# Performance work log

Hardware: AMD Instinct MI355X
Metric: run time of the kernel (lower is better)

## Reference

```python
import jax, jax.numpy as jnp
import numpy as np

N, C, NE = 65536, 128, 10
INV_SQ2 = float(1.0 / np.sqrt(2.0))   # path weight sqrt(ir_out.dim / n_paths) * w3j, 0e outputs
INV_SQ6 = float(1.0 / np.sqrt(6.0))   # sqrt(1/2) * 1/sqrt(3) for the 1o.1o->0e dot path


def _fcn(x, weights):
    # e3nn FullyConnectedNet: no biases, fan-in normalized, silu between layers
    h = x
    for i, W in enumerate(weights):
        h = (h @ W) * float(1.0 / np.sqrt(W.shape[0]))
        if i < len(weights) - 1:
            h = jax.nn.silu(h)
    return h


def setup_inputs() -> dict:
    key = jax.random.key(0)
    ks = jax.random.split(key, 24)
    elem = jax.random.randint(ks[0], (N,), 0, NE)
    return {
        'node_feats_s': jax.random.normal(ks[1], (N, C), jnp.float32),
        'node_feats_v': jax.random.normal(ks[2], (N, C, 3), jnp.float32),
        'sc': jax.random.normal(ks[3], (N, 4 * C), jnp.float32),
        'node_attrs': jax.nn.one_hot(elem, NE, dtype=jnp.float32),
        'magmom_node_inv_feats': jax.random.normal(ks[4], (N, 16), jnp.float32),
        'magmom_node_attrs': jax.random.normal(ks[5], (N, 4), jnp.float32),
        'magmom_lenghts': jax.random.uniform(ks[6], (N, 1), jnp.float32),
        'Ws': jax.random.normal(ks[7], (NE, 5, C), jnp.float32),
        'Wv': jax.random.normal(ks[8], (NE, 4, C), jnp.float32),
        'Wc1': jax.random.normal(ks[9], (16, 64), jnp.float32),
        'Wc2': jax.random.normal(ks[10], (64, 64), jnp.float32),
        'Wc3': jax.random.normal(ks[11], (64, 64), jnp.float32),
        'Wc4': jax.random.normal(ks[12], (64, 4 * C), jnp.float32),
        'Wb1': jax.random.normal(ks[13], (16, 64), jnp.float32),
        'Wb2': jax.random.normal(ks[14], (64, 64), jnp.float32),
        'Wb3': jax.random.normal(ks[15], (64, 64), jnp.float32),
        'Wb4': jax.random.normal(ks[16], (64, C), jnp.float32),
        'exp_scaling': jnp.full((1,), 5.0, jnp.float32),
        'Wl0': jax.random.normal(ks[17], (2 * C, C), jnp.float32),
        'Wl1': jax.random.normal(ks[18], (2 * C, C), jnp.float32),
        'Wo0': jax.random.normal(ks[19], (C, C), jnp.float32),
        'Wo1': jax.random.normal(ks[20], (C, C), jnp.float32),
    }


def reference(node_feats_s, node_feats_v, sc, node_attrs, magmom_node_inv_feats,
              magmom_node_attrs, magmom_lenghts, Ws, Wv, Wc1, Wc2, Wc3, Wc4,
              Wb1, Wb2, Wb3, Wb4, exp_scaling, Wl0, Wl1, Wo0, Wo1):
    s, v = node_feats_s, node_feats_v                     # [N,C], [N,C,3]
    # --- SymmetricContraction (correlation 3, l<=1): per-element weighted symmetric CG basis ---
    ws = jnp.einsum('ne,epc->npc', node_attrs, Ws)        # [N,5,C] element-selected weights
    wv = jnp.einsum('ne,epc->npc', node_attrs, Wv)        # [N,4,C]
    vv = jnp.sum(v * v, axis=-1)                          # [N,C] invariant |v|^2
    out_s = (ws[:, 0] * s + ws[:, 1] * (s * s) + ws[:, 2] * vv
             + ws[:, 3] * (s * s * s) + ws[:, 4] * (s * vv))
    gate = wv[:, 0] + wv[:, 1] * s + wv[:, 2] * (s * s) + wv[:, 3] * vv
    out_v = gate[..., None] * v                           # [N,C,3] all 1o basis terms are multiples of v
    # --- conv_tp weights from invariant magmom feats ---
    tp_w = _fcn(magmom_node_inv_feats, [Wc1, Wc2, Wc3, Wc4])   # [N,4C]
    w0, w1, w2, w3 = (tp_w[:, 0:C], tp_w[:, C:2 * C], tp_w[:, 2 * C:3 * C], tp_w[:, 3 * C:4 * C])
    y0 = magmom_node_attrs[:, 0:1]                        # 1x0e
    y1 = magmom_node_attrs[:, 1:4]                        # 1x1o
    # --- path-sparse TensorProduct (uvu, per-sample weights), 4 instructions ---
    m0 = INV_SQ2 * w0 * out_s * y0                                     # 0e x 0e -> 0e
    m1 = INV_SQ6 * w1 * jnp.einsum('nci,ni->nc', out_v, y1)           # 1o x 1o -> 0e
    m2 = INV_SQ2 * w2[..., None] * out_s[..., None] * y1[:, None, :]  # 0e x 1o -> 1o
    m3 = INV_SQ2 * w3[..., None] * out_v * y0[:, :, None]             # 1o x 0e -> 1o
    # --- one-body magmom basis added to the scalar channels ---
    ob = _fcn(magmom_node_inv_feats, [Wb1, Wb2, Wb3, Wb4])            # [N,C]
    m0 = m0 + (1.0 - jnp.exp(-exp_scaling * magmom_lenghts)) * ob
    # --- equivariant Linear(irreps_mid -> target) + Linear(target -> target) + sc ---
    scal = jnp.concatenate([m0, m1], axis=1)              # [N,2C] 0e block
    vecs = jnp.concatenate([m2, m3], axis=1)              # [N,2C,3] 1o block
    inv_2c = float(1.0 / np.sqrt(2 * C))
    inv_c = float(1.0 / np.sqrt(C))
    out0 = (scal @ Wl0) * inv_2c
    out1 = jnp.einsum('nci,co->noi', vecs, Wl1) * inv_2c
    o0 = (out_s @ Wo0) * inv_c
    o1 = jnp.einsum('nci,co->noi', out_v, Wo1) * inv_c
    msg0 = out0 + o0 + sc[:, :C]
    msg1 = (out1 + o1).reshape(-1, 3 * C) + sc[:, C:]
    return jnp.concatenate([msg0, msg1], axis=1)          # [N, 4C] = target_irreps.dim
```

## Files before the change

### kernel.cpp

```cpp
#include <hip/hip_runtime.h>

#define NNODES 65536
#define CC 128
#define NEL 10
#define BN 32
#define NT 256

#define INV_SQ2f 0.70710678118654752440f
#define INV_SQ6f 0.40824829046386301637f
#define INV_2Cf  0.0625f
#define INV_Cf   0.08838834764831845f
#define S16f 0.25f
#define S64f 0.125f

#define WS_FRAGS 312
#define WS_BYTES (WS_FRAGS * 1024)

typedef __attribute__((ext_vector_type(8))) short s16x8;
typedef __attribute__((ext_vector_type(4))) float f32x4;
#define MFMA16(a, b, c) __builtin_amdgcn_mfma_f32_16x16x32_bf16((a), (b), (c), 0, 0, 0)

union U8 { unsigned short u[8]; s16x8 s; };

__device__ __forceinline__ unsigned short bf16rne(float x) {
    unsigned int u = __float_as_uint(x);
    return (unsigned short)((u + 0x7FFFu + ((u >> 16) & 1u)) >> 16);
}
__device__ __forceinline__ float bf2f(unsigned short h) {
    return __uint_as_float(((unsigned int)h) << 16);
}
__device__ __forceinline__ unsigned int packbf(float a, float b) {
    return (unsigned int)bf16rne(a) | (((unsigned int)bf16rne(b)) << 16);
}
__device__ __forceinline__ float siluf(float x) {
    return x * (1.0f / (1.0f + __expf(-x)));
}

extern "C" __global__ void prep_frags(
    const float* __restrict__ WC1, const float* __restrict__ WC2,
    const float* __restrict__ WC3, const float* __restrict__ WB1,
    const float* __restrict__ WB2, const float* __restrict__ WB3,
    const float* __restrict__ WC4, const float* __restrict__ WB4,
    const float* __restrict__ WL0, const float* __restrict__ WO0,
    const float* __restrict__ WL1, const float* __restrict__ WO1,
    unsigned short* __restrict__ wsb)
{
    const int b = blockIdx.x;
    const int l = threadIdx.x;
    const float* W; int K, N, nKS, base; float sc;
    if      (b <  4) { W = WC1; K = 16;  N = 64;  nKS = 1; base = 0;   sc = S16f; }
    else if (b < 12) { W = WC2; K = 64;  N = 64;  nKS = 2; base = 4;   sc = S64f; }
    else if (b < 20) { W = WC3; K = 64;  N = 64;  nKS = 2; base = 12;  sc = S64f; }
    else if (b < 24) { W = WB1; K = 16;  N = 64;  nKS = 1; base = 20;  sc = S16f; }
    else if (b < 32) { W = WB2; K = 64;  N = 64;  nKS = 2; base = 24;  sc = S64f; }
    else if (b < 40) { W = WB3; K = 64;  N = 64;  nKS = 2; base = 32;  sc = S64f; }
    else if (b < 104){ W = WC4; K = 64;  N = 512; nKS = 2; base = 40;  sc = S64f; }
    else if (b < 120){ W = WB4; K = 64;  N = 128; nKS = 2; base = 104; sc = S64f; }
    else if (b < 184){ W = WL0; K = 256; N = 128; nKS = 8; base = 120; sc = INV_2Cf; }
    else if (b < 216){ W = WO0; K = 128; N = 128; nKS = 4; base = 184; sc = INV_Cf; }
    else if (b < 280){ W = WL1; K = 256; N = 128; nKS = 8; base = 216; sc = INV_2Cf; }
    else             { W = WO1; K = 128; N = 128; nKS = 4; base = 280; sc = INV_Cf; }
    const int f  = b - base;
    const int nt = f / nKS, ks = f % nKS;
    const int n  = nt * 16 + (l & 15);
    const int k0 = ks * 32 + (l >> 4) * 8;
    U8 v;
    #pragma unroll
    for (int j = 0; j < 8; ++j) {
        const int k = k0 + j;
        const float x = (k < K) ? W[(size_t)k * N + n] * sc : 0.0f;
        v.u[j] = bf16rne(x);
    }
    *(s16x8*)(wsb + (size_t)b * 512 + l * 8) = v.s;
}

__device__ __forceinline__ s16x8 ldB(const unsigned short* __restrict__ wsb, int fragidx, int lane) {
    return *(const s16x8*)(wsb + ((size_t)fragidx << 9) + lane * 8);
}
__device__ __forceinline__ s16x8 ldA136(const unsigned short* X, int row, int ks, int gq) {
    return *(const s16x8*)(X + row * 136 + ks * 32 + gq * 8);
}
__device__ __forceinline__ s16x8 ldA72(const unsigned short* X, int row, int ks, int gq) {
    return *(const s16x8*)(X + row * 72 + ks * 32 + gq * 8);
}

extern "C" __global__ void __launch_bounds__(NT)
epb_mfma(const float* __restrict__ Sin, const float* __restrict__ Vin,
         const float* __restrict__ SCp, const float* __restrict__ ATT,
         const float* __restrict__ INVF, const float* __restrict__ MNA,
         const float* __restrict__ MLEN, const float* __restrict__ WSp,
         const float* __restrict__ WVp, const float* __restrict__ ESC,
         const unsigned short* __restrict__ wsb, float* __restrict__ OUT)
{
    extern __shared__ char smem[];
    unsigned short* B1 = (unsigned short*)smem;
    unsigned short* B2 = B1 + 4352;
    unsigned short* B3 = B2 + 4352;
    unsigned short* B4 = B3 + 4352;
    unsigned short* B5 = B4 + 4352;
    unsigned short* B6 = B5 + 4352;
    float* y0f  = (float*)(smem + 6 * 8704);
    float* y1f  = y0f + 32;
    float* etf  = y1f + 96;
    int*   eidx = (int*)(etf + 32);

    const int tid  = threadIdx.x;
    const int n0   = blockIdx.x * BN;
    const int w    = tid >> 6;
    const int lane = tid & 63;
    const int cl   = lane & 15;
    const int gq   = lane >> 4;
    const f32x4 Z4 = {0.f, 0.f, 0.f, 0.f};

    U8 invu[2];
    #pragma unroll
    for (int rg = 0; rg < 2; ++rg) {
        if (gq < 2) {
            const float* ip = INVF + (size_t)(n0 + rg * 16 + cl) * 16 + gq * 8;
            #pragma unroll
            for (int j = 0; j < 8; ++j) invu[rg].u[j] = bf16rne(ip[j]);
        } else {
            #pragma unroll
            for (int j = 0; j < 8; ++j) invu[rg].u[j] = 0;
        }
    }

    if (tid < BN) {
        const int gn = n0 + tid;
        y0f[tid] = MNA[gn * 4 + 0];
        y1f[tid * 3 + 0] = MNA[gn * 4 + 1];
        y1f[tid * 3 + 1] = MNA[gn * 4 + 2];
        y1f[tid * 3 + 2] = MNA[gn * 4 + 3];
        etf[tid] = 1.0f - __expf(-ESC[0] * MLEN[gn]);
        int e = 0;
        #pragma unroll
        for (int k = 0; k < NEL; ++k)
            if (ATT[(size_t)gn * NEL + k] > 0.5f) e = k;
        eidx[tid] = e;
    }

    #pragma unroll
    for (int rg = 0; rg < 2; ++rg) {
        const f32x4 c = MFMA16(invu[rg].s, ldB(wsb, 0 + w, lane), Z4);
        const f32x4 b = MFMA16(invu[rg].s, ldB(wsb, 20 + w, lane), Z4);
        #pragma unroll
        for (int r = 0; r < 4; ++r) {
            const int rw = rg * 16 + gq * 4 + r;
            B1[rw * 72 + w * 16 + cl] = bf16rne(siluf(c[r]));
            B2[rw * 72 + w * 16 + cl] = bf16rne(siluf(b[r]));
        }
    }
    __syncthreads();

    {
        f32x4 c[2] = {Z4, Z4}, b[2] = {Z4, Z4};
        #pragma unroll
        for (int ks = 0; ks < 2; ++ks) {
            const s16x8 fc = ldB(wsb, 4 + w * 2 + ks, lane);
            const s16x8 fb = ldB(wsb, 24 + w * 2 + ks, lane);
            #pragma unroll
            for (int rg = 0; rg < 2; ++rg) {
                c[rg] = MFMA16(ldA72(B1, rg * 16 + cl, ks, gq), fc, c[rg]);
                b[rg] = MFMA16(ldA72(B2, rg * 16 + cl, ks, gq), fb, b[rg]);
            }
        }
        #pragma unroll
        for (int rg = 0; rg < 2; ++rg)
            #pragma unroll
            for (int r = 0; r < 4; ++r) {
                const int rw = rg * 16 + gq * 4 + r;
                B3[rw * 72 + w * 16 + cl] = bf16rne(siluf(c[rg][r]));
                B4[rw * 72 + w * 16 + cl] = bf16rne(siluf(b[rg][r]));
            }
    }
    __syncthreads();

    {
        f32x4 c[2] = {Z4, Z4}, b[2] = {Z4, Z4};
        #pragma unroll
        for (int ks = 0; ks < 2; ++ks) {
            const s16x8 fc = ldB(wsb, 12 + w * 2 + ks, lane);
            const s16x8 fb = ldB(wsb, 32 + w * 2 + ks, lane);
            #pragma unroll
            for (int rg = 0; rg < 2; ++rg) {
                c[rg] = MFMA16(ldA72(B3, rg * 16 + cl, ks, gq), fc, c[rg]);
                b[rg] = MFMA16(ldA72(B4, rg * 16 + cl, ks, gq), fb, b[rg]);
            }
        }
        #pragma unroll
        for (int rg = 0; rg < 2; ++rg)
            #pragma unroll
            for (int r = 0; r < 4; ++r) {
                const int rw = rg * 16 + gq * 4 + r;
                B5[rw * 72 + w * 16 + cl] = bf16rne(siluf(c[rg][r]));
                B6[rw * 72 + w * 16 + cl] = bf16rne(siluf(b[rg][r]));
            }
    }
    __syncthreads();

    s16x8 h3c[2][2], h3b[2][2];
    #pragma unroll
    for (int rg = 0; rg < 2; ++rg)
        #pragma unroll
        for (int ks = 0; ks < 2; ++ks) {
            h3c[rg][ks] = ldA72(B5, rg * 16 + cl, ks, gq);
            h3b[rg][ks] = ldA72(B6, rg * 16 + cl, ks, gq);
        }
    f32x4 obacc[2][2];
    #pragma unroll
    for (int tc = 0; tc < 2; ++tc) {
        const int T = w * 2 + tc;
        const s16x8 f0 = ldB(wsb, 104 + T * 2 + 0, lane);
        const s16x8 f1 = ldB(wsb, 104 + T * 2 + 1, lane);
        #pragma unroll
        for (int rg = 0; rg < 2; ++rg)
            obacc[rg][tc] = MFMA16(h3b[rg][1], f1, MFMA16(h3b[rg][0], f0, Z4));
    }

    unsigned int vpack[3][8];
    {
        const int row = tid >> 3;
        const int c0  = (tid & 7) << 4;
        const size_t gn = (size_t)(n0 + row);
        const float4 mna = *(const float4*)(MNA + gn * 4);
        const float y10 = mna.y, y11 = mna.z, y12 = mna.w;
        int e = 0;
        #pragma unroll
        for (int k = 0; k < NEL; ++k)
            if (ATT[gn * NEL + k] > 0.5f) e = k;
        const float* sp  = Sin + gn * CC + c0;
        const float* vp  = Vin + (gn * CC + c0) * 3;
        const float* wsp = WSp + ((size_t)e * 5) * CC + c0;
        const float* wvp = WVp + ((size_t)e * 4) * CC + c0;
        unsigned int* B1d = (unsigned int*)B1;
        unsigned int* B2d = (unsigned int*)B2;
        unsigned int* B3d = (unsigned int*)B3;
        const int dbase = row * 68 + (c0 >> 1);
        #pragma unroll
        for (int jp = 0; jp < 8; ++jp) {
            const int c = 2 * jp;
            const float2 s2 = *(const float2*)(sp + c);
            const float2 va = *(const float2*)(vp + 3 * c);
            const float2 vb = *(const float2*)(vp + 3 * c + 2);
            const float2 vc = *(const float2*)(vp + 3 * c + 4);
            vpack[0][jp] = packbf(va.x, vb.y);
            vpack[1][jp] = packbf(va.y, vc.x);
            vpack[2][jp] = packbf(vb.x, vc.y);
            const float vv0 = va.x * va.x + va.y * va.y + vb.x * vb.x;
            const float vv1 = vb.y * vb.y + vc.x * vc.x + vc.y * vc.y;
            const float vy0 = va.x * y10 + va.y * y11 + vb.x * y12;
            const float vy1 = vb.y * y10 + vc.x * y11 + vc.y * y12;
            const float2 p0 = *(const float2*)(wsp + 0 * CC + c);
            const float2 p1 = *(const float2*)(wsp + 1 * CC + c);
            const float2 p2 = *(const float2*)(wsp + 2 * CC + c);
            const float2 p3 = *(const float2*)(wsp + 3 * CC + c);
            const float2 p4 = *(const float2*)(wsp + 4 * CC + c);
            const float2 q0 = *(const float2*)(wvp + 0 * CC + c);
            const float2 q1 = *(const float2*)(wvp + 1 * CC + c);
            const float2 q2 = *(const float2*)(wvp + 2 * CC + c);
            const float2 q3 = *(const float2*)(wvp + 3 * CC + c);
            const float s0 = s2.x, s1 = s2.y;
            const float ss0 = s0 * s0, ss1 = s1 * s1;
            const float os0 = p0.x * s0 + p1.x * ss0 + p2.x * vv0 + p3.x * (ss0 * s0) + p4.x * (s0 * vv0);
            const float os1 = p0.y * s1 + p1.y * ss1 + p2.y * vv1 + p3.y * (ss1 * s1) + p4.y * (s1 * vv1);
            const float gt0 = q0.x + q1.x * s0 + q2.x * ss0 + q3.x * vv0;
            const float gt1 = q0.y + q1.y * s1 + q2.y * ss1 + q3.y * vv1;
            B1d[dbase + jp] = packbf(os0, os1);
            B2d[dbase + jp] = packbf(gt0, gt1);
            B3d[dbase + jp] = packbf(vy0, vy1);
        }
    }
    __syncthreads();

#define WCHUNK(q, wc)                                                          \
    {                                                                          \
        _Pragma("unroll")                                                      \
        for (int tc = 0; tc < 2; ++tc) {                                       \
            const int T = w * 2 + tc;                                          \
            const s16x8 f0 = ldB(wsb, 40 + ((q) * 8 + T) * 2 + 0, lane);       \
            const s16x8 f1 = ldB(wsb, 40 + ((q) * 8 + T) * 2 + 1, lane);       \
            _Pragma("unroll")                                                  \
            for (int rg = 0; rg < 2; ++rg)                                     \
                wc[rg][tc] = MFMA16(h3c[rg][1], f1, MFMA16(h3c[rg][0], f0, Z4)); \
        }                                                                      \
    }
    {
        f32x4 wc[2][2];
        WCHUNK(0, wc)
        #pragma unroll
        for (int rg = 0; rg < 2; ++rg)
            #pragma unroll
            for (int tc = 0; tc < 2; ++tc)
                #pragma unroll
                for (int r = 0; r < 4; ++r) {
                    const int rw = rg * 16 + gq * 4 + r;
                    const int col = (w * 2 + tc) * 16 + cl;
                    const float os = bf2f(B1[rw * 136 + col]);
                    B4[rw * 136 + col] = bf16rne(INV_SQ2f * wc[rg][tc][r] * os * y0f[rw]
                                                 + etf[rw] * obacc[rg][tc][r]);
                }
        WCHUNK(1, wc)
        #pragma unroll
        for (int rg = 0; rg < 2; ++rg)
            #pragma unroll
            for (int tc = 0; tc < 2; ++tc)
                #pragma unroll
                for (int r = 0; r < 4; ++r) {
                    const int rw = rg * 16 + gq * 4 + r;
                    const int col = (w * 2 + tc) * 16 + cl;
                    const float gt = bf2f(B2[rw * 136 + col]);
                    const float vy = bf2f(B3[rw * 136 + col]);
                    B3[rw * 136 + col] = bf16rne(INV_SQ6f * wc[rg][tc][r] * gt * vy);
                }
        WCHUNK(2, wc)
        #pragma unroll
        for (int rg = 0; rg < 2; ++rg)
            #pragma unroll
            for (int tc = 0; tc < 2; ++tc)
                #pragma unroll
                for (int r = 0; r < 4; ++r) {
                    const int rw = rg * 16 + gq * 4 + r;
                    const int col = (w * 2 + tc) * 16 + cl;
                    B6[rw * 136 + col] = bf16rne(INV_SQ2f * wc[rg][tc][r] * bf2f(B1[rw * 136 + col]));
                }
        WCHUNK(3, wc)
        #pragma unroll
        for (int rg = 0; rg < 2; ++rg)
            #pragma unroll
            for (int tc = 0; tc < 2; ++tc)
                #pragma unroll
                for (int r = 0; r < 4; ++r) {
                    const int rw = rg * 16 + gq * 4 + r;
                    const int col = (w * 2 + tc) * 16 + cl;
                    const float gt = bf2f(B2[rw * 136 + col]);
                    B5[rw * 136 + col] = bf16rne(INV_SQ2f * wc[rg][tc][r] * gt * y0f[rw]);
                }
    }
#undef WCHUNK
    __syncthreads();

    f32x4 tacc[2][2] = {{Z4, Z4}, {Z4, Z4}};
    {
        f32x4 acc[2][2] = {{Z4, Z4}, {Z4, Z4}};
        #pragma unroll
        for (int ks = 0; ks < 12; ++ks) {
            const unsigned short* Xa = (ks < 4) ? B4 : (ks < 8) ? B3 : B1;
            s16x8 a[2];
            #pragma unroll
            for (int rg = 0; rg < 2; ++rg) a[rg] = ldA136(Xa, rg * 16 + cl, ks & 3, gq);
            #pragma unroll
            for (int tc = 0; tc < 2; ++tc) {
                const int T = w * 2 + tc;
                const int fi = (ks < 8) ? (120 + T * 8 + ks) : (184 + T * 4 + (ks - 8));
                const s16x8 bfrag = ldB(wsb, fi, lane);
                #pragma unroll
                for (int rg = 0; rg < 2; ++rg)
                    acc[rg][tc] = MFMA16(a[rg], bfrag, acc[rg][tc]);
            }
        }
        #pragma unroll
        for (int ks = 0; ks < 4; ++ks) {
            s16x8 a[2];
            #pragma unroll
            for (int rg = 0; rg < 2; ++rg) a[rg] = ldA136(B6, rg * 16 + cl, ks, gq);
            #pragma unroll
            for (int tc = 0; tc < 2; ++tc) {
                const s16x8 bfrag = ldB(wsb, 216 + (w * 2 + tc) * 8 + ks, lane);
                #pragma unroll
                for (int rg = 0; rg < 2; ++rg)
                    tacc[rg][tc] = MFMA16(a[rg], bfrag, tacc[rg][tc]);
            }
        }
        #pragma unroll
        for (int rg = 0; rg < 2; ++rg)
            #pragma unroll
            for (int tc = 0; tc < 2; ++tc)
                #pragma unroll
                for (int r = 0; r < 4; ++r) {
                    const int rw = rg * 16 + gq * 4 + r;
                    const size_t o = (size_t)(n0 + rw) * 512 + (w * 2 + tc) * 16 + cl;
                    OUT[o] = acc[rg][tc][r] + SCp[o];
                }
    }
    __syncthreads();

    f32x4 acc3[3][2][2];

#define STAGE_I(i, DSTB, DSTG)                                                  \
    {                                                                           \
        const int dbase = (tid >> 3) * 68 + (tid & 7) * 8;                      \
        const unsigned int* bD = (const unsigned int*)B5;                       \
        const unsigned int* gD = (const unsigned int*)B2;                       \
        unsigned int* o1 = (unsigned int*)(DSTB);                               \
        unsigned int* o3 = (unsigned int*)(DSTG);                               \
        _Pragma("unroll")                                                       \
        for (int jp = 0; jp < 8; ++jp) {                                        \
            const unsigned int bd = bD[dbase + jp];                             \
            const unsigned int gd = gD[dbase + jp];                             \
            const float v0 = bf2f((unsigned short)(vpack[i][jp] & 0xffff));     \
            const float v1 = bf2f((unsigned short)(vpack[i][jp] >> 16));        \
            o1[dbase + jp] = packbf(bf2f((unsigned short)(bd & 0xffff)) * v0,   \
                                    bf2f((unsigned short)(bd >> 16)) * v1);     \
            o3[dbase + jp] = packbf(bf2f((unsigned short)(gd & 0xffff)) * v0,   \
                                    bf2f((unsigned short)(gd >> 16)) * v1);     \
        }                                                                       \
    }

#define GEMM_I(i, SRCB, SRCG)                                                   \
    {                                                                           \
        _Pragma("unroll")                                                       \
        for (int rg = 0; rg < 2; ++rg)                                          \
            _Pragma("unroll")                                                   \
            for (int tc = 0; tc < 2; ++tc) acc3[i][rg][tc] = Z4;                \
        _Pragma("unroll")                                                       \
        for (int ks = 0; ks < 4; ++ks) {                                        \
            s16x8 a1[2], a3[2];                                                 \
            _Pragma("unroll")                                                   \
            for (int rg = 0; rg < 2; ++rg) {                                    \
                a1[rg] = ldA136((SRCB), rg * 16 + cl, ks, gq);                  \
                a3[rg] = ldA136((SRCG), rg * 16 + cl, ks, gq);                  \
            }                                                                   \
            _Pragma("unroll")                                                   \
            for (int tc = 0; tc < 2; ++tc) {                                    \
                const int T = w * 2 + tc;                                       \
                const s16x8 fb = ldB(wsb, 216 + T * 8 + 4 + ks, lane);          \
                const s16x8 fg = ldB(wsb, 280 + T * 4 + ks, lane);              \
                _Pragma("unroll")                                               \
                for (int rg = 0; rg < 2; ++rg) {                                \
                    acc3[i][rg][tc] = MFMA16(a1[rg], fb, acc3[i][rg][tc]);      \
                    acc3[i][rg][tc] = MFMA16(a3[rg], fg, acc3[i][rg][tc]);      \
                }                                                               \
            }                                                                   \
        }                                                                       \
    }

    STAGE_I(0, B1, B3)
    __syncthreads();
    GEMM_I(0, B1, B3)
    STAGE_I(1, B4, B6)
    __syncthreads();
    GEMM_I(1, B4, B6)
    STAGE_I(2, B1, B3)
    __syncthreads();
    GEMM_I(2, B1, B3)

    #pragma unroll
    for (int rg = 0; rg < 2; ++rg)
        #pragma unroll
        for (int tc = 0; tc < 2; ++tc)
            #pragma unroll
            for (int r = 0; r < 4; ++r) {
                const int rw = rg * 16 + gq * 4 + r;
                const int col = (w * 2 + tc) * 16 + cl;
                const size_t o = (size_t)(n0 + rw) * 512 + 128 + (size_t)col * 3;
                const float tv = tacc[rg][tc][r];
                OUT[o + 0] = acc3[0][rg][tc][r] + tv * y1f[rw * 3 + 0] + SCp[o + 0];
                OUT[o + 1] = acc3[1][rg][tc][r] + tv * y1f[rw * 3 + 1] + SCp[o + 1];
                OUT[o + 2] = acc3[2][rg][tc][r] + tv * y1f[rw * 3 + 2] + SCp[o + 2];
            }
#undef STAGE_I
#undef GEMM_I
}

extern "C" void kernel_launch(void* const* d_in, const int* in_sizes, int n_in,
                              void* d_out, int out_size, void* d_ws, size_t ws_size,
                              hipStream_t stream)
{
    (void)in_sizes; (void)n_in; (void)out_size; (void)ws_size;
    const float* Sin  = (const float*)d_in[0];
    const float* Vin  = (const float*)d_in[1];
    const float* SCp  = (const float*)d_in[2];
    const float* ATT  = (const float*)d_in[3];
    const float* INVF = (const float*)d_in[4];
    const float* MNA  = (const float*)d_in[5];
    const float* MLEN = (const float*)d_in[6];
    const float* WSp  = (const float*)d_in[7];
    const float* WVp  = (const float*)d_in[8];
    const float* WC1  = (const float*)d_in[9];
    const float* WC2  = (const float*)d_in[10];
    const float* WC3  = (const float*)d_in[11];
    const float* WC4  = (const float*)d_in[12];
    const float* WB1  = (const float*)d_in[13];
    const float* WB2  = (const float*)d_in[14];
    const float* WB3  = (const float*)d_in[15];
    const float* WB4  = (const float*)d_in[16];
    const float* ESC  = (const float*)d_in[17];
    const float* WL0  = (const float*)d_in[18];
    const float* WL1  = (const float*)d_in[19];
    const float* WO0  = (const float*)d_in[20];
    const float* WO1  = (const float*)d_in[21];
    float* OUT = (float*)d_out;

    unsigned short* wsb = (unsigned short*)d_ws;
    hipLaunchKernelGGL(prep_frags, dim3(WS_FRAGS), dim3(64), 0, stream,
                       WC1, WC2, WC3, WB1, WB2, WB3, WC4, WB4,
                       WL0, WO0, WL1, WO1, wsb);
    const size_t shbytes = (size_t)(6 * 8704 + 768);
    hipLaunchKernelGGL(epb_mfma, dim3(NNODES / BN), dim3(NT), shbytes, stream,
                       Sin, Vin, SCp, ATT, INVF, MNA, MLEN, WSp, WVp, ESC,
                       wsb, OUT);
}
```

Measured before the change: 166.4 us.

## Split the magmom MLP into a separate kernel writing h3 to workspace

Moves the two 3-layer radial/one-body MLPs out of the main fused kernel into a new mlp_h3 kernel. It runs one wave per 16 nodes with per-wave ping-pong LDS and no block barriers, and writes bf16 hidden activations to global workspace. The main kernel then loads h3 from global memory instead of computing it, which removes three __syncthreads phases and their LDS traffic. In exchange it adds an extra launch and about 16 MB of global write plus read, and it falls back to the old fused kernel when the workspace is too small.

```diff
diff --git a/kernel.cpp b/kernel.cpp
--- a/kernel.cpp
+++ b/kernel.cpp
@@ -14,7 +14,8 @@
 #define S64f 0.125f
 
 #define WS_FRAGS 312
-#define WS_BYTES (WS_FRAGS * 1024)
+#define H3_OFF   (WS_FRAGS * 512)
+#define WS_NEED  ((size_t)H3_OFF * 2 + (size_t)NNODES * 128 * 2)
 
 typedef __attribute__((ext_vector_type(8))) short s16x8;
 typedef __attribute__((ext_vector_type(4))) float f32x4;
@@ -84,13 +85,79 @@
     return *(const s16x8*)(X + row * 72 + ks * 32 + gq * 8);
 }
 
+extern "C" __global__ void __launch_bounds__(256)
+mlp_h3(const float* __restrict__ INVF, const unsigned short* __restrict__ wsb,
+       unsigned short* __restrict__ h3g)
+{
+    extern __shared__ unsigned short slab_all[];
+    const int tid  = threadIdx.x;
+    const int v    = tid >> 6;
+    const int lane = tid & 63;
+    const int cl   = lane & 15;
+    const int gq   = lane >> 4;
+    const int nbase = blockIdx.x * 64 + v * 16;
+    unsigned short* ping = slab_all + v * 2560;
+    unsigned short* pong = ping + 1280;
+    const f32x4 Z4 = {0.f, 0.f, 0.f, 0.f};
+
+    U8 invu;
+    if (gq < 2) {
+        const float* ip = INVF + (size_t)(nbase + cl) * 16 + gq * 8;
+        #pragma unroll
+        for (int j = 0; j < 8; ++j) invu.u[j] = bf16rne(ip[j]);
+    } else {
+        #pragma unroll
+        for (int j = 0; j < 8; ++j) invu.u[j] = 0;
+    }
+
+    #pragma unroll
+    for (int ch = 0; ch < 2; ++ch) {
+        #pragma unroll
+        for (int mt = 0; mt < 4; ++mt) {
+            const f32x4 c = MFMA16(invu.s, ldB(wsb, (ch ? 20 : 0) + mt, lane), Z4);
+            #pragma unroll
+            for (int r = 0; r < 4; ++r)
+                ping[(gq * 4 + r) * 80 + mt * 16 + cl] = bf16rne(siluf(c[r]));
+        }
+        #pragma unroll
+        for (int mt = 0; mt < 4; ++mt) {
+            f32x4 c = Z4;
+            #pragma unroll
+            for (int ks = 0; ks < 2; ++ks)
+                c = MFMA16(*(const s16x8*)(ping + cl * 80 + ks * 32 + gq * 8),
+                           ldB(wsb, (ch ? 24 : 4) + mt * 2 + ks, lane), c);
+            #pragma unroll
+            for (int r = 0; r < 4; ++r)
+                pong[(gq * 4 + r) * 80 + mt * 16 + cl] = bf16rne(siluf(c[r]));
+        }
+        #pragma unroll
+        for (int mt = 0; mt < 4; ++mt) {
+            f32x4 c = Z4;
+            #pragma unroll
+            for (int ks = 0; ks < 2; ++ks)
+                c = MFMA16(*(const s16x8*)(pong + cl * 80 + ks * 32 + gq * 8),
+                           ldB(wsb, (ch ? 32 : 12) + mt * 2 + ks, lane), c);
+            #pragma unroll
+            for (int r = 0; r < 4; ++r)
+                ping[(gq * 4 + r) * 80 + mt * 16 + cl] = bf16rne(siluf(c[r]));
+        }
+        #pragma unroll
+        for (int it = 0; it < 2; ++it) {
+            const int idx = it * 64 + lane;
+            const int row = idx >> 3, seg = idx & 7;
+            *(s16x8*)(h3g + (size_t)(nbase + row) * 128 + ch * 64 + seg * 8) =
+                *(const s16x8*)(ping + row * 80 + seg * 8);
+        }
+    }
+}
+
 extern "C" __global__ void __launch_bounds__(NT)
-epb_mfma(const float* __restrict__ Sin, const float* __restrict__ Vin,
+epb_lean(const float* __restrict__ Sin, const float* __restrict__ Vin,
          const float* __restrict__ SCp, const float* __restrict__ ATT,
-         const float* __restrict__ INVF, const float* __restrict__ MNA,
-         const float* __restrict__ MLEN, const float* __restrict__ WSp,
-         const float* __restrict__ WVp, const float* __restrict__ ESC,
-         const unsigned short* __restrict__ wsb, float* __restrict__ OUT)
+         const float* __restrict__ MNA, const float* __restrict__ MLEN,
+         const float* __restrict__ WSp, const float* __restrict__ WVp,
+         const float* __restrict__ ESC, const unsigned short* __restrict__ wsb,
+         const unsigned short* __restrict__ h3g, float* __restrict__ OUT)
 {
     extern __shared__ char smem[];
     unsigned short* B1 = (unsigned short*)smem;
@@ -102,7 +169,6 @@
     float* y0f  = (float*)(smem + 6 * 8704);
     float* y1f  = y0f + 32;
     float* etf  = y1f + 96;
-    int*   eidx = (int*)(etf + 32);
 
     const int tid  = threadIdx.x;
     const int n0   = blockIdx.x * BN;
@@ -112,19 +178,6 @@
     const int gq   = lane >> 4;
     const f32x4 Z4 = {0.f, 0.f, 0.f, 0.f};
 
-    U8 invu[2];
-    #pragma unroll
-    for (int rg = 0; rg < 2; ++rg) {
-        if (gq < 2) {
-            const float* ip = INVF + (size_t)(n0 + rg * 16 + cl) * 16 + gq * 8;
-            #pragma unroll
-            for (int j = 0; j < 8; ++j) invu[rg].u[j] = bf16rne(ip[j]);
-        } else {
-            #pragma unroll
-            for (int j = 0; j < 8; ++j) invu[rg].u[j] = 0;
-        }
-    }
-
     if (tid < BN) {
         const int gn = n0 + tid;
         y0f[tid] = MNA[gn * 4 + 0];
@@ -132,79 +185,16 @@
         y1f[tid * 3 + 1] = MNA[gn * 4 + 2];
         y1f[tid * 3 + 2] = MNA[gn * 4 + 3];
         etf[tid] = 1.0f - __expf(-ESC[0] * MLEN[gn]);
-        int e = 0;
-        #pragma unroll
-        for (int k = 0; k < NEL; ++k)
-            if (ATT[(size_t)gn * NEL + k] > 0.5f) e = k;
-        eidx[tid] = e;
-    }
-
-    #pragma unroll
-    for (int rg = 0; rg < 2; ++rg) {
-        const f32x4 c = MFMA16(invu[rg].s, ldB(wsb, 0 + w, lane), Z4);
-        const f32x4 b = MFMA16(invu[rg].s, ldB(wsb, 20 + w, lane), Z4);
-        #pragma unroll
-        for (int r = 0; r < 4; ++r) {
-            const int rw = rg * 16 + gq * 4 + r;
-            B1[rw * 72 + w * 16 + cl] = bf16rne(siluf(c[r]));
-            B2[rw * 72 + w * 16 + cl] = bf16rne(siluf(b[r]));
-        }
-    }
-    __syncthreads();
-
-    {
-        f32x4 c[2] = {Z4, Z4}, b[2] = {Z4, Z4};
+    }
+
+    s16x8 h3c[2][2], h3b[2][2];
+    #pragma unroll
+    for (int rg = 0; rg < 2; ++rg)
         #pragma unroll
         for (int ks = 0; ks < 2; ++ks) {
-            const s16x8 fc = ldB(wsb, 4 + w * 2 + ks, lane);
-            const s16x8 fb = ldB(wsb, 24 + w * 2 + ks, lane);
-            #pragma unroll
-            for (int rg = 0; rg < 2; ++rg) {
-                c[rg] = MFMA16(ldA72(B1, rg * 16 + cl, ks, gq), fc, c[rg]);
-                b[rg] = MFMA16(ldA72(B2, rg * 16 + cl, ks, gq), fb, b[rg]);
-            }
-        }
-        #pragma unroll
-        for (int rg = 0; rg < 2; ++rg)
-            #pragma unroll
-            for (int r = 0; r < 4; ++r) {
-                const int rw = rg * 16 + gq * 4 + r;
-                B3[rw * 72 + w * 16 + cl] = bf16rne(siluf(c[rg][r]));
-                B4[rw * 72 + w * 16 + cl] = bf16rne(siluf(b[rg][r]));
-            }
-    }
-    __syncthreads();
-
-    {
-        f32x4 c[2] = {Z4, Z4}, b[2] = {Z4, Z4};
-        #pragma unroll
-        for (int ks = 0; ks < 2; ++ks) {
-            const s16x8 fc = ldB(wsb, 12 + w * 2 + ks, lane);
-            const s16x8 fb = ldB(wsb, 32 + w * 2 + ks, lane);
-            #pragma unroll
-            for (int rg = 0; rg < 2; ++rg) {
-                c[rg] = MFMA16(ldA72(B3, rg * 16 + cl, ks, gq), fc, c[rg]);
-                b[rg] = MFMA16(ldA72(B4, rg * 16 + cl, ks, gq), fb, b[rg]);
-            }
-        }
-        #pragma unroll
-        for (int rg = 0; rg < 2; ++rg)
-            #pragma unroll
-            for (int r = 0; r < 4; ++r) {
-                const int rw = rg * 16 + gq * 4 + r;
-                B5[rw * 72 + w * 16 + cl] = bf16rne(siluf(c[rg][r]));
-                B6[rw * 72 + w * 16 + cl] = bf16rne(siluf(b[rg][r]));
-            }
-    }
-    __syncthreads();
-
-    s16x8 h3c[2][2], h3b[2][2];
-    #pragma unroll
-    for (int rg = 0; rg < 2; ++rg)
-        #pragma unroll
-        for (int ks = 0; ks < 2; ++ks) {
-            h3c[rg][ks] = ldA72(B5, rg * 16 + cl, ks, gq);
-            h3b[rg][ks] = ldA72(B6, rg * 16 + cl, ks, gq);
+            const size_t base = (size_t)(n0 + rg * 16 + cl) * 128 + ks * 32 + gq * 8;
+            h3c[rg][ks] = *(const s16x8*)(h3g + base);
+            h3b[rg][ks] = *(const s16x8*)(h3g + base + 64);
         }
     f32x4 obacc[2][2];
     #pragma unroll
@@ -462,11 +452,370 @@
 #undef GEMM_I
 }
 
+extern "C" __global__ void __launch_bounds__(NT)
+epb_mfma(const float* __restrict__ Sin, const float* __restrict__ Vin,
+         const float* __restrict__ SCp, const float* __restrict__ ATT,
+         const float* __restrict__ INVF, const float* __restrict__ MNA,
+         const float* __restrict__ MLEN, const float* __restrict__ WSp,
+         const float* __restrict__ WVp, const float* __restrict__ ESC,
+         const unsigned short* __restrict__ wsb, float* __restrict__ OUT)
+{
+    extern __shared__ char smem[];
+    unsigned short* B1 = (unsigned short*)smem;
+    unsigned short* B2 = B1 + 4352;
+    unsigned short* B3 = B2 + 4352;
+    unsigned short* B4 = B3 + 4352;
+    unsigned short* B5 = B4 + 4352;
+    unsigned short* B6 = B5 + 4352;
+    float* y0f  = (float*)(smem + 6 * 8704);
+    float* y1f  = y0f + 32;
+    float* etf  = y1f + 96;
+
+    const int tid  = threadIdx.x;
+    const int n0   = blockIdx.x * BN;
+    const int w    = tid >> 6;
+    const int lane = tid & 63;
+    const int cl   = lane & 15;
+    const int gq   = lane >> 4;
+    const f32x4 Z4 = {0.f, 0.f, 0.f, 0.f};
+
+    U8 invu[2];
+    #pragma unroll
+    for (int rg = 0; rg < 2; ++rg) {
+        if (gq < 2) {
+            const float* ip = INVF + (size_t)(n0 + rg * 16 + cl) * 16 + gq * 8;
+            #pragma unroll
+            for (int j = 0; j < 8; ++j) invu[rg].u[j] = bf16rne(ip[j]);
+        } else {
+            #pragma unroll
+            for (int j = 0; j < 8; ++j) invu[rg].u[j] = 0;
+        }
+    }
+    if (tid < BN) {
+        const int gn = n0 + tid;
+        y0f[tid] = MNA[gn * 4 + 0];
+        y1f[tid * 3 + 0] = MNA[gn * 4 + 1];
+        y1f[tid * 3 + 1] = MNA[gn * 4 + 2];
+        y1f[tid * 3 + 2] = MNA[gn * 4 + 3];
+        etf[tid] = 1.0f - __expf(-ESC[0] * MLEN[gn]);
+    }
+    #pragma unroll
+    for (int rg = 0; rg < 2; ++rg) {
+        const f32x4 c = MFMA16(invu[rg].s, ldB(wsb, 0 + w, lane), Z4);
+        const f32x4 b = MFMA16(invu[rg].s, ldB(wsb, 20 + w, lane), Z4);
+        #pragma unroll
+        for (int r = 0; r < 4; ++r) {
+            const int rw = rg * 16 + gq * 4 + r;
+            B1[rw * 72 + w * 16 + cl] = bf16rne(siluf(c[r]));
+            B2[rw * 72 + w * 16 + cl] = bf16rne(siluf(b[r]));
+        }
+    }
+    __syncthreads();
+    {
+        f32x4 c[2] = {Z4, Z4}, b[2] = {Z4, Z4};
+        #pragma unroll
+        for (int ks = 0; ks < 2; ++ks) {
+            const s16x8 fc = ldB(wsb, 4 + w * 2 + ks, lane);
+            const s16x8 fb = ldB(wsb, 24 + w * 2 + ks, lane);
+            #pragma unroll
+            for (int rg = 0; rg < 2; ++rg) {
+                c[rg] = MFMA16(ldA72(B1, rg * 16 + cl, ks, gq), fc, c[rg]);
+                b[rg] = MFMA16(ldA72(B2, rg * 16 + cl, ks, gq), fb, b[rg]);
+            }
+        }
+        #pragma unroll
+        for (int rg = 0; rg < 2; ++rg)
+            #pragma unroll
+            for (int r = 0; r < 4; ++r) {
+                const int rw = rg * 16 + gq * 4 + r;
+                B3[rw * 72 + w * 16 + cl] = bf16rne(siluf(c[rg][r]));
+                B4[rw * 72 + w * 16 + cl] = bf16rne(siluf(b[rg][r]));
+            }
+    }
+    __syncthreads();
+    {
+        f32x4 c[2] = {Z4, Z4}, b[2] = {Z4, Z4};
+        #pragma unroll
+        for (int ks = 0; ks < 2; ++ks) {
+            const s16x8 fc = ldB(wsb, 12 + w * 2 + ks, lane);
+            const s16x8 fb = ldB(wsb, 32 + w * 2 + ks, lane);
+            #pragma unroll
+            for (int rg = 0; rg < 2; ++rg) {
+                c[rg] = MFMA16(ldA72(B3, rg * 16 + cl, ks, gq), fc, c[rg]);
+                b[rg] = MFMA16(ldA72(B4, rg * 16 + cl, ks, gq), fb, b[rg]);
+            }
+        }
+        #pragma unroll
+        for (int rg = 0; rg < 2; ++rg)
+            #pragma unroll
+            for (int r = 0; r < 4; ++r) {
+                const int rw = rg * 16 + gq * 4 + r;
+                B5[rw * 72 + w * 16 + cl] = bf16rne(siluf(c[rg][r]));
+                B6[rw * 72 + w * 16 + cl] = bf16rne(siluf(b[rg][r]));
+            }
+    }
+    __syncthreads();
+    s16x8 h3c[2][2], h3b[2][2];
+    #pragma unroll
+    for (int rg = 0; rg < 2; ++rg)
+        #pragma unroll
+        for (int ks = 0; ks < 2; ++ks) {
+            h3c[rg][ks] = ldA72(B5, rg * 16 + cl, ks, gq);
+            h3b[rg][ks] = ldA72(B6, rg * 16 + cl, ks, gq);
+        }
+    f32x4 obacc[2][2];
+    #pragma unroll
+    for (int tc = 0; tc < 2; ++tc) {
+        const int T = w * 2 + tc;
+        const s16x8 f0 = ldB(wsb, 104 + T * 2 + 0, lane);
+        const s16x8 f1 = ldB(wsb, 104 + T * 2 + 1, lane);
+        #pragma unroll
+        for (int rg = 0; rg < 2; ++rg)
+            obacc[rg][tc] = MFMA16(h3b[rg][1], f1, MFMA16(h3b[rg][0], f0, Z4));
+    }
+    unsigned int vpack[3][8];
+    {
+        const int row = tid >> 3;
+        const int c0  = (tid & 7) << 4;
+        const size_t gn = (size_t)(n0 + row);
+        const float4 mna = *(const float4*)(MNA + gn * 4);
+        const float y10 = mna.y, y11 = mna.z, y12 = mna.w;
+        int e = 0;
+        #pragma unroll
+        for (int k = 0; k < NEL; ++k)
+            if (ATT[gn * NEL + k] > 0.5f) e = k;
+        const float* sp  = Sin + gn * CC + c0;
+        const float* vp  = Vin + (gn * CC + c0) * 3;
+        const float* wsp = WSp + ((size_t)e * 5) * CC + c0;
+        const float* wvp = WVp + ((size_t)e * 4) * CC + c0;
+        unsigned int* B1d = (unsigned int*)B1;
+        unsigned int* B2d = (unsigned int*)B2;
+        unsigned int* B3d = (unsigned int*)B3;
+        const int dbase = row * 68 + (c0 >> 1);
+        #pragma unroll
+        for (int jp = 0; jp < 8; ++jp) {
+            const int c = 2 * jp;
+            const float2 s2 = *(const float2*)(sp + c);
+            const float2 va = *(const float2*)(vp + 3 * c);
+            const float2 vb = *(const float2*)(vp + 3 * c + 2);
+            const float2 vc = *(const float2*)(vp + 3 * c + 4);
+            vpack[0][jp] = packbf(va.x, vb.y);
+            vpack[1][jp] = packbf(va.y, vc.x);
+            vpack[2][jp] = packbf(vb.x, vc.y);
+            const float vv0 = va.x * va.x + va.y * va.y + vb.x * vb.x;
+            const float vv1 = vb.y * vb.y + vc.x * vc.x + vc.y * vc.y;
+            const float vy0 = va.x * y10 + va.y * y11 + vb.x * y12;
+            const float vy1 = vb.y * y10 + vc.x * y11 + vc.y * y12;
+            const float2 p0 = *(const float2*)(wsp + 0 * CC + c);
+            const float2 p1 = *(const float2*)(wsp + 1 * CC + c);
+            const float2 p2 = *(const float2*)(wsp + 2 * CC + c);
+            const float2 p3 = *(const float2*)(wsp + 3 * CC + c);
+            const float2 p4 = *(const float2*)(wsp + 4 * CC + c);
+            const float2 q0 = *(const float2*)(wvp + 0 * CC + c);
+            const float2 q1 = *(const float2*)(wvp + 1 * CC + c);
+            const float2 q2 = *(const float2*)(wvp + 2 * CC + c);
+            const float2 q3 = *(const float2*)(wvp + 3 * CC + c);
+            const float s0 = s2.x, s1 = s2.y;
+            const float ss0 = s0 * s0, ss1 = s1 * s1;
+            const float os0 = p0.x * s0 + p1.x * ss0 + p2.x * vv0 + p3.x * (ss0 * s0) + p4.x * (s0 * vv0);
+            const float os1 = p0.y * s1 + p1.y * ss1 + p2.y * vv1 + p3.y * (ss1 * s1) + p4.y * (s1 * vv1);
+            const float gt0 = q0.x + q1.x * s0 + q2.x * ss0 + q3.x * vv0;
+            const float gt1 = q0.y + q1.y * s1 + q2.y * ss1 + q3.y * vv1;
+            B1d[dbase + jp] = packbf(os0, os1);
+            B2d[dbase + jp] = packbf(gt0, gt1);
+            B3d[dbase + jp] = packbf(vy0, vy1);
+        }
+    }
+    __syncthreads();
+#define WCHUNK(q, wc)                                                          \
+    {                                                                          \
+        _Pragma("unroll")                                                      \
+        for (int tc = 0; tc < 2; ++tc) {                                       \
+            const int T = w * 2 + tc;                                          \
+            const s16x8 f0 = ldB(wsb, 40 + ((q) * 8 + T) * 2 + 0, lane);       \
+            const s16x8 f1 = ldB(wsb, 40 + ((q) * 8 + T) * 2 + 1, lane);       \
+            _Pragma("unroll")                                                  \
+            for (int rg = 0; rg < 2; ++rg)                                     \
+                wc[rg][tc] = MFMA16(h3c[rg][1], f1, MFMA16(h3c[rg][0], f0, Z4)); \
+        }                                                                      \
+    }
+    {
+        f32x4 wc[2][2];
+        WCHUNK(0, wc)
+        #pragma unroll
+        for (int rg = 0; rg < 2; ++rg)
+            #pragma unroll
+            for (int tc = 0; tc < 2; ++tc)
+                #pragma unroll
+                for (int r = 0; r < 4; ++r) {
+                    const int rw = rg * 16 + gq * 4 + r;
+                    const int col = (w * 2 + tc) * 16 + cl;
+                    const float os = bf2f(B1[rw * 136 + col]);
+                    B4[rw * 136 + col] = bf16rne(INV_SQ2f * wc[rg][tc][r] * os * y0f[rw]
+                                                 + etf[rw] * obacc[rg][tc][r]);
+                }
+        WCHUNK(1, wc)
+        #pragma unroll
+        for (int rg = 0; rg < 2; ++rg)
+            #pragma unroll
+            for (int tc = 0; tc < 2; ++tc)
+                #pragma unroll
+                for (int r = 0; r < 4; ++r) {
+                    const int rw = rg * 16 + gq * 4 + r;
+                    const int col = (w * 2 + tc) * 16 + cl;
+                    const float gt = bf2f(B2[rw * 136 + col]);
+                    const float vy = bf2f(B3[rw * 136 + col]);
+                    B3[rw * 136 + col] = bf16rne(INV_SQ6f * wc[rg][tc][r] * gt * vy);
+                }
+        WCHUNK(2, wc)
+        #pragma unroll
+        for (int rg = 0; rg < 2; ++rg)
+            #pragma unroll
+            for (int tc = 0; tc < 2; ++tc)
+                #pragma unroll
+                for (int r = 0; r < 4; ++r) {
+                    const int rw = rg * 16 + gq * 4 + r;
+                    const int col = (w * 2 + tc) * 16 + cl;
+                    B6[rw * 136 + col] = bf16rne(INV_SQ2f * wc[rg][tc][r] * bf2f(B1[rw * 136 + col]));
+                }
+        WCHUNK(3, wc)
+        #pragma unroll
+        for (int rg = 0; rg < 2; ++rg)
+            #pragma unroll
+            for (int tc = 0; tc < 2; ++tc)
+                #pragma unroll
+                for (int r = 0; r < 4; ++r) {
+                    const int rw = rg * 16 + gq * 4 + r;
+                    const int col = (w * 2 + tc) * 16 + cl;
+                    const float gt = bf2f(B2[rw * 136 + col]);
+                    B5[rw * 136 + col] = bf16rne(INV_SQ2f * wc[rg][tc][r] * gt * y0f[rw]);
+                }
+    }
+#undef WCHUNK
+    __syncthreads();
+    f32x4 tacc[2][2] = {{Z4, Z4}, {Z4, Z4}};
+    {
+        f32x4 acc[2][2] = {{Z4, Z4}, {Z4, Z4}};
+        #pragma unroll
+        for (int ks = 0; ks < 12; ++ks) {
+            const unsigned short* Xa = (ks < 4) ? B4 : (ks < 8) ? B3 : B1;
+            s16x8 a[2];
+            #pragma unroll
+            for (int rg = 0; rg < 2; ++rg) a[rg] = ldA136(Xa, rg * 16 + cl, ks & 3, gq);
+            #pragma unroll
+            for (int tc = 0; tc < 2; ++tc) {
+                const int T = w * 2 + tc;
+                const int fi = (ks < 8) ? (120 + T * 8 + ks) : (184 + T * 4 + (ks - 8));
+                const s16x8 bfrag = ldB(wsb, fi, lane);
+                #pragma unroll
+                for (int rg = 0; rg < 2; ++rg)
+                    acc[rg][tc] = MFMA16(a[rg], bfrag, acc[rg][tc]);
+            }
+        }
+        #pragma unroll
+        for (int ks = 0; ks < 4; ++ks) {
+            s16x8 a[2];
+            #pragma unroll
+            for (int rg = 0; rg < 2; ++rg) a[rg] = ldA136(B6, rg * 16 + cl, ks, gq);
+            #pragma unroll
+            for (int tc = 0; tc < 2; ++tc) {
+                const s16x8 bfrag = ldB(wsb, 216 + (w * 2 + tc) * 8 + ks, lane);
+                #pragma unroll
+                for (int rg = 0; rg < 2; ++rg)
+                    tacc[rg][tc] = MFMA16(a[rg], bfrag, tacc[rg][tc]);
+            }
+        }
+        #pragma unroll
+        for (int rg = 0; rg < 2; ++rg)
+            #pragma unroll
+            for (int tc = 0; tc < 2; ++tc)
+                #pragma unroll
+                for (int r = 0; r < 4; ++r) {
+                    const int rw = rg * 16 + gq * 4 + r;
+                    const size_t o = (size_t)(n0 + rw) * 512 + (w * 2 + tc) * 16 + cl;
+                    OUT[o] = acc[rg][tc][r] + SCp[o];
+                }
+    }
+    __syncthreads();
+    f32x4 acc3[3][2][2];
+#define STAGE_I(i, DSTB, DSTG)                                                  \
+    {                                                                           \
+        const int dbase = (tid >> 3) * 68 + (tid & 7) * 8;                      \
+        const unsigned int* bD = (const unsigned int*)B5;                       \
+        const unsigned int* gD = (const unsigned int*)B2;                       \
+        unsigned int* o1 = (unsigned int*)(DSTB);                               \
+        unsigned int* o3 = (unsigned int*)(DSTG);                               \
+        _Pragma("unroll")                                                       \
+        for (int jp = 0; jp < 8; ++jp) {                                        \
+            const unsigned int bd = bD[dbase + jp];                             \
+            const unsigned int gd = gD[dbase + jp];                             \
+            const float v0 = bf2f((unsigned short)(vpack[i][jp] & 0xffff));     \
+            const float v1 = bf2f((unsigned short)(vpack[i][jp] >> 16));        \
+            o1[dbase + jp] = packbf(bf2f((unsigned short)(bd & 0xffff)) * v0,   \
+                                    bf2f((unsigned short)(bd >> 16)) * v1);     \
+            o3[dbase + jp] = packbf(bf2f((unsigned short)(gd & 0xffff)) * v0,   \
+                                    bf2f((unsigned short)(gd >> 16)) * v1);     \
+        }                                                                       \
+    }
+#define GEMM_I(i, SRCB, SRCG)                                                   \
+    {                                                                           \
+        _Pragma("unroll")                                                       \
+        for (int rg = 0; rg < 2; ++rg)                                          \
+            _Pragma("unroll")                                                   \
+            for (int tc = 0; tc < 2; ++tc) acc3[i][rg][tc] = Z4;                \
+        _Pragma("unroll")                                                       \
+        for (int ks = 0; ks < 4; ++ks) {                                        \
+            s16x8 a1[2], a3[2];                                                 \
+            _Pragma("unroll")                                                   \
+            for (int rg = 0; rg < 2; ++rg) {                                    \
+                a1[rg] = ldA136((SRCB), rg * 16 + cl, ks, gq);                  \
+                a3[rg] = ldA136((SRCG), rg * 16 + cl, ks, gq);                  \
+            }                                                                   \
+            _Pragma("unroll")                                                   \
+            for (int tc = 0; tc < 2; ++tc) {                                    \
+                const int T = w * 2 + tc;                                       \
+                const s16x8 fb = ldB(wsb, 216 + T * 8 + 4 + ks, lane);          \
+                const s16x8 fg = ldB(wsb, 280 + T * 4 + ks, lane);              \
+                _Pragma("unroll")                                               \
+                for (int rg = 0; rg < 2; ++rg) {                                \
+                    acc3[i][rg][tc] = MFMA16(a1[rg], fb, acc3[i][rg][tc]);      \
+                    acc3[i][rg][tc] = MFMA16(a3[rg], fg, acc3[i][rg][tc]);      \
+                }                                                               \
+            }                                                                   \
+        }                                                                       \
+    }
+    STAGE_I(0, B1, B3)
+    __syncthreads();
+    GEMM_I(0, B1, B3)
+    STAGE_I(1, B4, B6)
+    __syncthreads();
+    GEMM_I(1, B4, B6)
+    STAGE_I(2, B1, B3)
+    __syncthreads();
+    GEMM_I(2, B1, B3)
+    #pragma unroll
+    for (int rg = 0; rg < 2; ++rg)
+        #pragma unroll
+        for (int tc = 0; tc < 2; ++tc)
+            #pragma unroll
+            for (int r = 0; r < 4; ++r) {
+                const int rw = rg * 16 + gq * 4 + r;
+                const int col = (w * 2 + tc) * 16 + cl;
+                const size_t o = (size_t)(n0 + rw) * 512 + 128 + (size_t)col * 3;
+                const float tv = tacc[rg][tc][r];
+                OUT[o + 0] = acc3[0][rg][tc][r] + tv * y1f[rw * 3 + 0] + SCp[o + 0];
+                OUT[o + 1] = acc3[1][rg][tc][r] + tv * y1f[rw * 3 + 1] + SCp[o + 1];
+                OUT[o + 2] = acc3[2][rg][tc][r] + tv * y1f[rw * 3 + 2] + SCp[o + 2];
+            }
+#undef STAGE_I
+#undef GEMM_I
+}
+
 extern "C" void kernel_launch(void* const* d_in, const int* in_sizes, int n_in,
                               void* d_out, int out_size, void* d_ws, size_t ws_size,
                               hipStream_t stream)
 {
-    (void)in_sizes; (void)n_in; (void)out_size; (void)ws_size;
+    (void)in_sizes; (void)n_in; (void)out_size;
     const float* Sin  = (const float*)d_in[0];
     const float* Vin  = (const float*)d_in[1];
     const float* SCp  = (const float*)d_in[2];
@@ -496,7 +845,16 @@
                        WC1, WC2, WC3, WB1, WB2, WB3, WC4, WB4,
                        WL0, WO0, WL1, WO1, wsb);
     const size_t shbytes = (size_t)(6 * 8704 + 768);
-    hipLaunchKernelGGL(epb_mfma, dim3(NNODES / BN), dim3(NT), shbytes, stream,
-                       Sin, Vin, SCp, ATT, INVF, MNA, MLEN, WSp, WVp, ESC,
-                       wsb, OUT);
-}
+    if (ws_size >= WS_NEED) {
+        unsigned short* h3g = wsb + H3_OFF;
+        hipLaunchKernelGGL(mlp_h3, dim3(NNODES / 64), dim3(256), 20480, stream,
+                           INVF, wsb, h3g);
+        hipLaunchKernelGGL(epb_lean, dim3(NNODES / BN), dim3(NT), shbytes, stream,
+                           Sin, Vin, SCp, ATT, MNA, MLEN, WSp, WVp, ESC,
+                           wsb, h3g, OUT);
+    } else {
+        hipLaunchKernelGGL(epb_mfma, dim3(NNODES / BN), dim3(NT), shbytes, stream,
+                           Sin, Vin, SCp, ATT, INVF, MNA, MLEN, WSp, WVp, ESC,
+                           wsb, OUT);
+    }
+}
```

Measured after the change: 195.3 us. +17.4%, slower.

## Cut LDS from six to four staging buffers to raise occupancy

Applied to the files above, without the earlier changes.

Drops two of the six shared-memory staging buffers (B5, B6) and the unused eidx array, aliasing their contents onto B1–B4 and reordering the WCHUNK 2/3 products and the tacc GEMM after the main scalar GEMM. The goal is to shrink per-block LDS from about 53KB to about 35KB so more blocks fit per CU. In exchange the kernel needs several extra __syncthreads barriers to protect the reused buffers, and keeps the wc2/wc3 accumulators live in registers longer, which can raise register pressure.

```diff
diff --git a/kernel.cpp b/kernel.cpp
--- a/kernel.cpp
+++ b/kernel.cpp
@@ -14,7 +14,6 @@
 #define S64f 0.125f
 
 #define WS_FRAGS 312
-#define WS_BYTES (WS_FRAGS * 1024)
 
 typedef __attribute__((ext_vector_type(8))) short s16x8;
 typedef __attribute__((ext_vector_type(4))) float f32x4;
@@ -97,12 +96,9 @@
     unsigned short* B2 = B1 + 4352;
     unsigned short* B3 = B2 + 4352;
     unsigned short* B4 = B3 + 4352;
-    unsigned short* B5 = B4 + 4352;
-    unsigned short* B6 = B5 + 4352;
-    float* y0f  = (float*)(smem + 6 * 8704);
+    float* y0f  = (float*)(smem + 4 * 8704);
     float* y1f  = y0f + 32;
     float* etf  = y1f + 96;
-    int*   eidx = (int*)(etf + 32);
 
     const int tid  = threadIdx.x;
     const int n0   = blockIdx.x * BN;
@@ -132,11 +128,6 @@
         y1f[tid * 3 + 1] = MNA[gn * 4 + 2];
         y1f[tid * 3 + 2] = MNA[gn * 4 + 3];
         etf[tid] = 1.0f - __expf(-ESC[0] * MLEN[gn]);
-        int e = 0;
-        #pragma unroll
-        for (int k = 0; k < NEL; ++k)
-            if (ATT[(size_t)gn * NEL + k] > 0.5f) e = k;
-        eidx[tid] = e;
     }
 
     #pragma unroll
@@ -187,13 +178,14 @@
                 b[rg] = MFMA16(ldA72(B4, rg * 16 + cl, ks, gq), fb, b[rg]);
             }
         }
+        __syncthreads();
         #pragma unroll
         for (int rg = 0; rg < 2; ++rg)
             #pragma unroll
             for (int r = 0; r < 4; ++r) {
                 const int rw = rg * 16 + gq * 4 + r;
-                B5[rw * 72 + w * 16 + cl] = bf16rne(siluf(c[rg][r]));
-                B6[rw * 72 + w * 16 + cl] = bf16rne(siluf(b[rg][r]));
+                B1[rw * 72 + w * 16 + cl] = bf16rne(siluf(c[rg][r]));
+                B2[rw * 72 + w * 16 + cl] = bf16rne(siluf(b[rg][r]));
             }
     }
     __syncthreads();
@@ -203,8 +195,8 @@
     for (int rg = 0; rg < 2; ++rg)
         #pragma unroll
         for (int ks = 0; ks < 2; ++ks) {
-            h3c[rg][ks] = ldA72(B5, rg * 16 + cl, ks, gq);
-            h3b[rg][ks] = ldA72(B6, rg * 16 + cl, ks, gq);
+            h3c[rg][ks] = ldA72(B1, rg * 16 + cl, ks, gq);
+            h3b[rg][ks] = ldA72(B2, rg * 16 + cl, ks, gq);
         }
     f32x4 obacc[2][2];
     #pragma unroll
@@ -216,6 +208,7 @@
         for (int rg = 0; rg < 2; ++rg)
             obacc[rg][tc] = MFMA16(h3b[rg][1], f1, MFMA16(h3b[rg][0], f0, Z4));
     }
+    __syncthreads();
 
     unsigned int vpack[3][8];
     {
@@ -284,6 +277,7 @@
                 wc[rg][tc] = MFMA16(h3c[rg][1], f1, MFMA16(h3c[rg][0], f0, Z4)); \
         }                                                                      \
     }
+
     {
         f32x4 wc[2][2];
         WCHUNK(0, wc)
@@ -312,35 +306,13 @@
                     const float vy = bf2f(B3[rw * 136 + col]);
                     B3[rw * 136 + col] = bf16rne(INV_SQ6f * wc[rg][tc][r] * gt * vy);
                 }
-        WCHUNK(2, wc)
-        #pragma unroll
-        for (int rg = 0; rg < 2; ++rg)
-            #pragma unroll
-            for (int tc = 0; tc < 2; ++tc)
-                #pragma unroll
-                for (int r = 0; r < 4; ++r) {
-                    const int rw = rg * 16 + gq * 4 + r;
-                    const int col = (w * 2 + tc) * 16 + cl;
-                    B6[rw * 136 + col] = bf16rne(INV_SQ2f * wc[rg][tc][r] * bf2f(B1[rw * 136 + col]));
-                }
-        WCHUNK(3, wc)
-        #pragma unroll
-        for (int rg = 0; rg < 2; ++rg)
-            #pragma unroll
-            for (int tc = 0; tc < 2; ++tc)
-                #pragma unroll
-                for (int r = 0; r < 4; ++r) {
-                    const int rw = rg * 16 + gq * 4 + r;
-                    const int col = (w * 2 + tc) * 16 + cl;
-                    const float gt = bf2f(B2[rw * 136 + col]);
-                    B5[rw * 136 + col] = bf16rne(INV_SQ2f * wc[rg][tc][r] * gt * y0f[rw]);
-                }
-    }
-#undef WCHUNK
-    __syncthreads();
-
-    f32x4 tacc[2][2] = {{Z4, Z4}, {Z4, Z4}};
+    }
+    __syncthreads();
+
+    f32x4 wc2[2][2], wc3[2][2];
     {
+        WCHUNK(2, wc2)
+        WCHUNK(3, wc3)
         f32x4 acc[2][2] = {{Z4, Z4}, {Z4, Z4}};
         #pragma unroll
         for (int ks = 0; ks < 12; ++ks) {
@@ -359,19 +331,6 @@
             }
         }
         #pragma unroll
-        for (int ks = 0; ks < 4; ++ks) {
-            s16x8 a[2];
-            #pragma unroll
-            for (int rg = 0; rg < 2; ++rg) a[rg] = ldA136(B6, rg * 16 + cl, ks, gq);
-            #pragma unroll
-            for (int tc = 0; tc < 2; ++tc) {
-                const s16x8 bfrag = ldB(wsb, 216 + (w * 2 + tc) * 8 + ks, lane);
-                #pragma unroll
-                for (int rg = 0; rg < 2; ++rg)
-                    tacc[rg][tc] = MFMA16(a[rg], bfrag, tacc[rg][tc]);
-            }
-        }
-        #pragma unroll
         for (int rg = 0; rg < 2; ++rg)
             #pragma unroll
             for (int tc = 0; tc < 2; ++tc)
@@ -383,16 +342,47 @@
                 }
     }
     __syncthreads();
+#undef WCHUNK
+
+    #pragma unroll
+    for (int rg = 0; rg < 2; ++rg)
+        #pragma unroll
+        for (int tc = 0; tc < 2; ++tc)
+            #pragma unroll
+            for (int r = 0; r < 4; ++r) {
+                const int rw = rg * 16 + gq * 4 + r;
+                const int col = (w * 2 + tc) * 16 + cl;
+                B4[rw * 136 + col] = bf16rne(INV_SQ2f * wc2[rg][tc][r] * bf2f(B1[rw * 136 + col]));
+                const float gt = bf2f(B2[rw * 136 + col]);
+                B3[rw * 136 + col] = bf16rne(INV_SQ2f * wc3[rg][tc][r] * gt * y0f[rw]);
+            }
+    __syncthreads();
+
+    f32x4 tacc[2][2] = {{Z4, Z4}, {Z4, Z4}};
+    #pragma unroll
+    for (int ks = 0; ks < 4; ++ks) {
+        s16x8 a[2];
+        #pragma unroll
+        for (int rg = 0; rg < 2; ++rg) a[rg] = ldA136(B4, rg * 16 + cl, ks, gq);
+        #pragma unroll
+        for (int tc = 0; tc < 2; ++tc) {
+            const s16x8 bfrag = ldB(wsb, 216 + (w * 2 + tc) * 8 + ks, lane);
+            #pragma unroll
+            for (int rg = 0; rg < 2; ++rg)
+                tacc[rg][tc] = MFMA16(a[rg], bfrag, tacc[rg][tc]);
+        }
+    }
+    __syncthreads();
 
     f32x4 acc3[3][2][2];
 
-#define STAGE_I(i, DSTB, DSTG)                                                  \
+#define STAGE_I(i)                                                              \
     {                                                                           \
         const int dbase = (tid >> 3) * 68 + (tid & 7) * 8;                      \
-        const unsigned int* bD = (const unsigned int*)B5;                       \
+        const unsigned int* bD = (const unsigned int*)B3;                       \
         const unsigned int* gD = (const unsigned int*)B2;                       \
-        unsigned int* o1 = (unsigned int*)(DSTB);                               \
-        unsigned int* o3 = (unsigned int*)(DSTG);                               \
+        unsigned int* o1 = (unsigned int*)B1;                                   \
+        unsigned int* o3 = (unsigned int*)B4;                                   \
         _Pragma("unroll")                                                       \
         for (int jp = 0; jp < 8; ++jp) {                                        \
             const unsigned int bd = bD[dbase + jp];                             \
@@ -406,7 +396,7 @@
         }                                                                       \
     }
 
-#define GEMM_I(i, SRCB, SRCG)                                                   \
+#define GEMM_I(i)                                                               \
     {                                                                           \
         _Pragma("unroll")                                                       \
         for (int rg = 0; rg < 2; ++rg)                                          \
@@ -417,8 +407,8 @@
             s16x8 a1[2], a3[2];                                                 \
             _Pragma("unroll")                                                   \
             for (int rg = 0; rg < 2; ++rg) {                                    \
-                a1[rg] = ldA136((SRCB), rg * 16 + cl, ks, gq);                  \
-                a3[rg] = ldA136((SRCG), rg * 16 + cl, ks, gq);                  \
+                a1[rg] = ldA136(B1, rg * 16 + cl, ks, gq);                      \
+                a3[rg] = ldA136(B4, rg * 16 + cl, ks, gq);                      \
             }                                                                   \
             _Pragma("unroll")                                                   \
             for (int tc = 0; tc < 2; ++tc) {                                    \
@@ -434,15 +424,17 @@
         }                                                                       \
     }
 
-    STAGE_I(0, B1, B3)
-    __syncthreads();
-    GEMM_I(0, B1, B3)
-    STAGE_I(1, B4, B6)
-    __syncthreads();
-    GEMM_I(1, B4, B6)
-    STAGE_I(2, B1, B3)
-    __syncthreads();
-    GEMM_I(2, B1, B3)
+    STAGE_I(0)
+    __syncthreads();
+    GEMM_I(0)
+    __syncthreads();
+    STAGE_I(1)
+    __syncthreads();
+    GEMM_I(1)
+    __syncthreads();
+    STAGE_I(2)
+    __syncthreads();
+    GEMM_I(2)
 
     #pragma unroll
     for (int rg = 0; rg < 2; ++rg)
@@ -495,7 +487,7 @@
     hipLaunchKernelGGL(prep_frags, dim3(WS_FRAGS), dim3(64), 0, stream,
                        WC1, WC2, WC3, WB1, WB2, WB3, WC4, WB4,
                        WL0, WO0, WL1, WO1, wsb);
-    const size_t shbytes = (size_t)(6 * 8704 + 768);
+    const size_t shbytes = (size_t)(4 * 8704 + 640);
     hipLaunchKernelGGL(epb_mfma, dim3(NNODES / BN), dim3(NT), shbytes, stream,
                        Sin, Vin, SCp, ATT, INVF, MNA, MLEN, WSp, WVp, ESC,
                        wsb, OUT);
```

Result: slower. 171.3 us (+3.0%).
